# Kernel tuning notes

Hardware: AMD Instinct MI355X
Metric: run time of the kernel (lower is better)

The kernel has to match this reference:

```python
import jax, jax.numpy as jnp
import numpy as np

NUM_GROUPS = 8   # num_groups1, recursive_index=False path
NUM_HEADS = 8


def setup_inputs() -> dict:
    key = jax.random.key(0)
    k1, k2, k3 = jax.random.split(key, 3)
    B, C, H, W = 4, 256, 64, 64
    x = jax.random.normal(k1, (B, C, H, W), dtype=jnp.float32)
    w_qkv = jax.random.normal(k2, (3 * C, C), dtype=jnp.float32) * 0.02
    w_proj = jax.random.normal(k3, (C, C), dtype=jnp.float32) * 0.02
    b_proj = jnp.zeros((C,), dtype=jnp.float32)
    return {"x": x, "w_qkv": w_qkv, "w_proj": w_proj, "b_proj": b_proj}


def reference(x, w_qkv, w_proj, b_proj):
    B, C, H, W = x.shape
    N = H * W
    G = NUM_GROUPS
    nh = NUM_HEADS
    hd = C // nh
    M = N // G
    scale = hd ** -0.5

    # b c h w -> b (h w) c
    xf = x.reshape(B, C, N).transpose(0, 2, 1)  # [B, N, C]

    # qkv linear (no bias), then split into groups / heads
    qkv = (xf @ w_qkv.T).reshape(B, G, M, 3, nh, hd)
    qkv = jnp.transpose(qkv, (3, 0, 1, 4, 2, 5))  # [3, B, G, nh, M, hd]
    q, k, v = qkv[0], qkv[1], qkv[2]

    # grouped multi-head attention, manual softmax
    attn = jax.nn.softmax(jnp.einsum('bghmd,bghnd->bghmn', q, k) * scale, axis=-1)
    out = jnp.einsum('bghmn,bghnd->bghmd', attn, v)

    # [B,G,nh,M,hd] -> [B,G,M,C] -> [B,N,C]
    out = out.transpose(0, 1, 3, 2, 4).reshape(B, N, C)

    out = out @ w_proj.T + b_proj

    # b (h w) c -> b c h w
    return out.transpose(0, 2, 1).reshape(B, C, H, W)
```

## Files before the change

### kernel.cpp

```cpp
#include <hip/hip_runtime.h>
#include <hip/hip_bf16.h>

#define Bb 4
#define Cc 256
#define Nn 4096
#define Gg 8
#define NHh 8
#define HDd 32
#define Mm 512

typedef __bf16 bf16_t;
typedef __bf16 bf16x2 __attribute__((ext_vector_type(2)));
typedef __bf16 bf16x8 __attribute__((ext_vector_type(8)));
typedef __bf16 bf16x4 __attribute__((ext_vector_type(4)));
typedef float f32x4 __attribute__((ext_vector_type(4)));

__device__ __forceinline__ void load_lds16(const bf16_t* g, bf16_t* l) {
  __builtin_amdgcn_global_load_lds(
      (const __attribute__((address_space(1))) void*)g,
      (__attribute__((address_space(3))) void*)l, 16, 0, 0);
}

__global__ __launch_bounds__(256) void prep_kernel(
    const float* __restrict__ x, bf16_t* __restrict__ xT,
    const float* __restrict__ wqkv, const float* __restrict__ wproj,
    bf16_t* __restrict__ wq_b, bf16_t* __restrict__ wp_b) {
  int bid = blockIdx.x, tid = threadIdx.x;
  if (bid >= 1024) {
    int i = (bid - 1024) * 256 + tid;
    wq_b[i] = (bf16_t)wqkv[i];
    if (i < Cc * Cc) wp_b[i] = (bf16_t)wproj[i];
    return;
  }
  __shared__ float t[64][65];
  int b = bid >> 8, c0 = ((bid >> 6) & 3) * 64, n0 = (bid & 63) * 64;
  const float* xp = x + ((long long)b * Cc + c0) * Nn + n0;
  for (int i = tid; i < 4096; i += 256) {
    int r = i >> 6, cc = i & 63;
    t[r][cc] = xp[(long long)r * Nn + cc];
  }
  __syncthreads();
  bf16_t* op = xT + ((long long)b * Nn + n0) * Cc + c0;
  for (int i = tid; i < 2048; i += 256) {
    int r = i >> 5, cc = (i & 31) * 2;
    bf16x2 w;
    w[0] = (bf16_t)t[cc][r];
    w[1] = (bf16_t)t[cc + 1][r];
    *(bf16x2*)&op[(long long)r * Cc + cc] = w;
  }
}

template <int MODE>
__global__ __launch_bounds__(256) void gemm_nt_kernel(
    const bf16_t* __restrict__ A, const bf16_t* __restrict__ Bt,
    void* __restrict__ C0, void* __restrict__ C1,
    const float* __restrict__ bias,
    int M, int N, int K, long long sB, long long sC) {
  __shared__ bf16_t As[128 * 32];
  __shared__ bf16_t Bs[128 * 32];
  int tid = threadIdx.x, lane = tid & 63, wid = tid >> 6;
  int quad = lane >> 4, l16 = lane & 15;
  int z = blockIdx.z;
  if (MODE != 1) Bt += sB * z;
  int m0 = blockIdx.y * 128, n0 = blockIdx.x * 128;
  int wm = (wid >> 1) * 64, wn = (wid & 1) * 64;

  f32x4 acc[4][4];
#pragma unroll
  for (int i = 0; i < 4; ++i)
#pragma unroll
    for (int j = 0; j < 4; ++j) acc[i][j] = (f32x4){0.f, 0.f, 0.f, 0.f};

  int scol = (lane & 3) * 8;
  for (int k0 = 0; k0 < K; k0 += 32) {
    __syncthreads();
#pragma unroll
    for (int r = 0; r < 2; ++r) {
      int chunk = wid * 2 + r;
      int row = chunk * 16 + (lane >> 2);
      load_lds16(&A[(long long)(m0 + row) * K + k0 + scol], &As[chunk * 512]);
      load_lds16(&Bt[(long long)(n0 + row) * K + k0 + scol], &Bs[chunk * 512]);
    }
    __syncthreads();
    bf16x8 a[4], b[4];
#pragma unroll
    for (int i = 0; i < 4; ++i)
      a[i] = *(const bf16x8*)&As[(wm + i * 16 + l16) * 32 + quad * 8];
#pragma unroll
    for (int j = 0; j < 4; ++j)
      b[j] = *(const bf16x8*)&Bs[(wn + j * 16 + l16) * 32 + quad * 8];
#pragma unroll
    for (int i = 0; i < 4; ++i)
#pragma unroll
      for (int j = 0; j < 4; ++j)
        acc[i][j] = __builtin_amdgcn_mfma_f32_16x16x32_bf16(a[i], b[j], acc[i][j], 0, 0, 0);
  }

#pragma unroll
  for (int i = 0; i < 4; ++i) {
#pragma unroll
    for (int j = 0; j < 4; ++j) {
      int col = n0 + wn + j * 16 + l16;
#pragma unroll
      for (int r = 0; r < 4; ++r) {
        int row = m0 + wm + i * 16 + quad * 4 + r;
        float v = acc[i][j][r];
        if (MODE == 1) {
          int b = row >> 12, g = (row >> 9) & 7, m = row & 511;
          int h = (col >> 5) & 7, d = col & 31;
          long long hb = (long long)((b << 6) | (g << 3) | h) * (Mm * HDd);
          if (col < 256)
            ((bf16_t*)C0)[hb + m * HDd + d] = (bf16_t)v;
          else
            ((bf16_t*)C1)[hb + m * HDd + d] = (bf16_t)v;
        } else if (MODE == 3) {
          int hh = row >> 5, d = row & 31, gg = col >> 9, m = col & 511;
          long long hb = (long long)((z << 6) | (gg << 3) | hh) * (Mm * HDd);
          ((bf16_t*)C0)[hb + d * Mm + m] = (bf16_t)v;
        } else {
          ((float*)C0)[sC * z + (long long)row * N + col] = v + bias[row];
        }
      }
    }
  }
}

__global__ __launch_bounds__(256, 2) void attn_kernel(
    const bf16_t* __restrict__ Qh, const bf16_t* __restrict__ Kh,
    const bf16_t* __restrict__ Vh, bf16_t* __restrict__ Oa) {
  __shared__ bf16_t Vs[32 * 520];
  int gid = blockIdx.x;
  int ms = gid & 1, head = gid >> 1;
  int h = head & 7, g = (head >> 3) & 7, b = head >> 6;
  int tid = threadIdx.x, lane = tid & 63, wid = tid >> 6;
  int quad = lane >> 4, l16 = lane & 15;
  const float ls = 0.17677669529663687f * 1.44269504088896340f;

  const bf16_t* Kg = Kh + (long long)head * (Mm * HDd);
  const bf16_t* Vg = Vh + (long long)head * (Mm * HDd);
  const bf16_t* Qg = Qh + (long long)head * (Mm * HDd) + ms * 256 * HDd;

#pragma unroll
  for (int it = 0; it < 8; ++it) {
    int d = wid * 8 + it;
    load_lds16(&Vg[d * Mm + lane * 8], &Vs[d * 520]);
  }
  __syncthreads();

  int rp0 = ((l16 >> 2) << 3) | (l16 & 3);
  const bf16_t* Kp0 = Kg + rp0 * HDd + quad * 8;
  const bf16_t* Kp1 = Kp0 + 4 * HDd;
  const bf16_t* VsL = &Vs[l16 * 520 + quad * 8];
  const bf16_t* VsH = &Vs[(16 + l16) * 520 + quad * 8];
  const f32x4 zero = (f32x4){0.f, 0.f, 0.f, 0.f};

#pragma unroll 1
  for (int t = 0; t < 4; ++t) {
    int m0 = wid * 64 + t * 16;
    bf16x8 qf = *(const bf16x8*)&Qg[(m0 + l16) * HDd + quad * 8];

    float sm = 0.f;
    f32x4 oL = zero, oH = zero;

#pragma unroll 4
    for (int c = 0; c < 16; ++c) {
      int nb = c * 32;
      bf16x8 kf0 = *(const bf16x8*)&Kp0[nb * HDd];
      bf16x8 kf1 = *(const bf16x8*)&Kp1[nb * HDd];
      f32x4 st0 = __builtin_amdgcn_mfma_f32_16x16x32_bf16(kf0, qf, zero, 0, 0, 0);
      f32x4 st1 = __builtin_amdgcn_mfma_f32_16x16x32_bf16(kf1, qf, zero, 0, 0, 0);
      bf16x8 pb;
#pragma unroll
      for (int r = 0; r < 4; ++r) {
        float e = __builtin_exp2f(st0[r] * ls);
        sm += e;
        pb[r] = (bf16_t)e;
      }
#pragma unroll
      for (int r = 0; r < 4; ++r) {
        float e = __builtin_exp2f(st1[r] * ls);
        sm += e;
        pb[4 + r] = (bf16_t)e;
      }
      bf16x8 vL = *(const bf16x8*)&VsL[nb];
      bf16x8 vH = *(const bf16x8*)&VsH[nb];
      oL = __builtin_amdgcn_mfma_f32_16x16x32_bf16(vL, pb, oL, 0, 0, 0);
      oH = __builtin_amdgcn_mfma_f32_16x16x32_bf16(vH, pb, oH, 0, 0, 0);
    }

    sm += __shfl_xor(sm, 16, 64);
    sm += __shfl_xor(sm, 32, 64);
    float inv = 1.f / sm;

    long long orow =
        ((long long)(b * Nn + g * Mm + ms * 256 + m0 + l16)) * Cc + h * HDd;
    bf16x4 wL, wH;
#pragma unroll
    for (int r = 0; r < 4; ++r) {
      wL[r] = (bf16_t)(oL[r] * inv);
      wH[r] = (bf16_t)(oH[r] * inv);
    }
    *(bf16x4*)&Oa[orow + quad * 4] = wL;
    *(bf16x4*)&Oa[orow + 16 + quad * 4] = wH;
  }
}

extern "C" void kernel_launch(void* const* d_in, const int* in_sizes, int n_in,
                              void* d_out, int out_size, void* d_ws, size_t ws_size,
                              hipStream_t stream) {
  (void)in_sizes; (void)n_in; (void)out_size; (void)ws_size;
  const float* x = (const float*)d_in[0];
  const float* w_qkv = (const float*)d_in[1];
  const float* w_proj = (const float*)d_in[2];
  const float* b_proj = (const float*)d_in[3];
  float* out = (float*)d_out;

  char* ws = (char*)d_ws;
  bf16_t* xT  = (bf16_t*)(ws);
  bf16_t* wqb = (bf16_t*)(ws + 8388608);
  bf16_t* wpb = (bf16_t*)(ws + 8781824);
  bf16_t* Qh  = (bf16_t*)(ws + 8912896);
  bf16_t* Kh  = (bf16_t*)(ws + 17301504);
  bf16_t* Vh  = (bf16_t*)(ws + 25690112);
  bf16_t* Oa  = (bf16_t*)(ws + 34078720);

  prep_kernel<<<1792, 256, 0, stream>>>(x, xT, w_qkv, w_proj, wqb, wpb);
  gemm_nt_kernel<1><<<dim3(4, 128, 1), 256, 0, stream>>>(
      xT, wqb, Qh, Kh, nullptr, Bb * Nn, 512, Cc, 0, 0);
  gemm_nt_kernel<3><<<dim3(32, 2, 4), 256, 0, stream>>>(
      wqb + 512 * Cc, xT, Vh, nullptr, nullptr, Cc, Nn, Cc,
      (long long)Nn * Cc, 0);
  attn_kernel<<<512, 256, 0, stream>>>(Qh, Kh, Vh, Oa);
  gemm_nt_kernel<2><<<dim3(32, 2, 4), 256, 0, stream>>>(
      wpb, Oa, out, nullptr, b_proj, Cc, Nn, Cc,
      (long long)Nn * Cc, (long long)Cc * Nn);
}
```

Measured before the change: 134.4 us.

## Merge QK and V GEMMs, fold softmax scale into Q, process two query tiles per wave

The separate QK and V projection GEMM launches become one 768-block kernel, which removes a launch and lets the two tile sets share the GPU. The softmax scale and log2(e) factor are now applied once when Q is written, so the attention inner loop no longer multiplies every score. The attention kernel now handles two 16-row query tiles per iteration, reusing each K fragment and V LDS read across both, at the cost of more accumulator registers. Rounding the scaled Q to bf16 slightly changes numerics.

```diff
diff --git a/kernel.cpp b/kernel.cpp
--- a/kernel.cpp
+++ b/kernel.cpp
@@ -11,9 +11,11 @@
 
 typedef __bf16 bf16_t;
 typedef __bf16 bf16x2 __attribute__((ext_vector_type(2)));
+typedef __bf16 bf16x4 __attribute__((ext_vector_type(4)));
 typedef __bf16 bf16x8 __attribute__((ext_vector_type(8)));
-typedef __bf16 bf16x4 __attribute__((ext_vector_type(4)));
 typedef float f32x4 __attribute__((ext_vector_type(4)));
+
+#define LSCALE (0.17677669529663687f * 1.44269504088896340f)
 
 __device__ __forceinline__ void load_lds16(const bf16_t* g, bf16_t* l) {
   __builtin_amdgcn_global_load_lds(
@@ -50,19 +52,31 @@
   }
 }
 
-template <int MODE>
-__global__ __launch_bounds__(256) void gemm_nt_kernel(
-    const bf16_t* __restrict__ A, const bf16_t* __restrict__ Bt,
-    void* __restrict__ C0, void* __restrict__ C1,
-    const float* __restrict__ bias,
-    int M, int N, int K, long long sB, long long sC) {
+__global__ __launch_bounds__(256) void qkv_gemm_kernel(
+    const bf16_t* __restrict__ xT, const bf16_t* __restrict__ wqb,
+    bf16_t* __restrict__ Qh, bf16_t* __restrict__ Kh, bf16_t* __restrict__ Vh) {
   __shared__ bf16_t As[128 * 32];
   __shared__ bf16_t Bs[128 * 32];
+  int bid = blockIdx.x;
   int tid = threadIdx.x, lane = tid & 63, wid = tid >> 6;
   int quad = lane >> 4, l16 = lane & 15;
-  int z = blockIdx.z;
-  if (MODE != 1) Bt += sB * z;
-  int m0 = blockIdx.y * 128, n0 = blockIdx.x * 128;
+  bool isQK = bid < 512;
+  const bf16_t *A, *Bt;
+  int m0, n0, z = 0;
+  if (isQK) {
+    m0 = (bid >> 2) * 128;
+    n0 = (bid & 3) * 128;
+    A = xT;
+    Bt = wqb;
+  } else {
+    int vb = bid - 512;
+    z = vb >> 6;
+    int rem = vb & 63;
+    m0 = (rem >> 5) * 128;
+    n0 = (rem & 31) * 128;
+    A = wqb + 512 * Cc;
+    Bt = xT + (long long)z * Nn * Cc;
+  }
   int wm = (wid >> 1) * 64, wn = (wid & 1) * 64;
 
   f32x4 acc[4][4];
@@ -72,14 +86,14 @@
     for (int j = 0; j < 4; ++j) acc[i][j] = (f32x4){0.f, 0.f, 0.f, 0.f};
 
   int scol = (lane & 3) * 8;
-  for (int k0 = 0; k0 < K; k0 += 32) {
+  for (int k0 = 0; k0 < Cc; k0 += 32) {
     __syncthreads();
 #pragma unroll
     for (int r = 0; r < 2; ++r) {
       int chunk = wid * 2 + r;
       int row = chunk * 16 + (lane >> 2);
-      load_lds16(&A[(long long)(m0 + row) * K + k0 + scol], &As[chunk * 512]);
-      load_lds16(&Bt[(long long)(n0 + row) * K + k0 + scol], &Bs[chunk * 512]);
+      load_lds16(&A[(long long)(m0 + row) * Cc + k0 + scol], &As[chunk * 512]);
+      load_lds16(&Bt[(long long)(n0 + row) * Cc + k0 + scol], &Bs[chunk * 512]);
     }
     __syncthreads();
     bf16x8 a[4], b[4];
@@ -105,20 +119,18 @@
       for (int r = 0; r < 4; ++r) {
         int row = m0 + wm + i * 16 + quad * 4 + r;
         float v = acc[i][j][r];
-        if (MODE == 1) {
-          int b = row >> 12, g = (row >> 9) & 7, m = row & 511;
-          int h = (col >> 5) & 7, d = col & 31;
-          long long hb = (long long)((b << 6) | (g << 3) | h) * (Mm * HDd);
+        if (isQK) {
+          int bb = row >> 12, gg = (row >> 9) & 7, m = row & 511;
+          int hh = (col >> 5) & 7, d = col & 31;
+          long long hb = (long long)((bb << 6) | (gg << 3) | hh) * (Mm * HDd);
           if (col < 256)
-            ((bf16_t*)C0)[hb + m * HDd + d] = (bf16_t)v;
+            Qh[hb + m * HDd + d] = (bf16_t)(v * LSCALE);
           else
-            ((bf16_t*)C1)[hb + m * HDd + d] = (bf16_t)v;
-        } else if (MODE == 3) {
+            Kh[hb + m * HDd + d] = (bf16_t)v;
+        } else {
           int hh = row >> 5, d = row & 31, gg = col >> 9, m = col & 511;
           long long hb = (long long)((z << 6) | (gg << 3) | hh) * (Mm * HDd);
-          ((bf16_t*)C0)[hb + d * Mm + m] = (bf16_t)v;
-        } else {
-          ((float*)C0)[sC * z + (long long)row * N + col] = v + bias[row];
+          Vh[hb + d * Mm + m] = (bf16_t)v;
         }
       }
     }
@@ -134,7 +146,6 @@
   int h = head & 7, g = (head >> 3) & 7, b = head >> 6;
   int tid = threadIdx.x, lane = tid & 63, wid = tid >> 6;
   int quad = lane >> 4, l16 = lane & 15;
-  const float ls = 0.17677669529663687f * 1.44269504088896340f;
 
   const bf16_t* Kg = Kh + (long long)head * (Mm * HDd);
   const bf16_t* Vg = Vh + (long long)head * (Mm * HDd);
@@ -155,53 +166,124 @@
   const f32x4 zero = (f32x4){0.f, 0.f, 0.f, 0.f};
 
 #pragma unroll 1
-  for (int t = 0; t < 4; ++t) {
-    int m0 = wid * 64 + t * 16;
-    bf16x8 qf = *(const bf16x8*)&Qg[(m0 + l16) * HDd + quad * 8];
-
-    float sm = 0.f;
-    f32x4 oL = zero, oH = zero;
+  for (int t = 0; t < 2; ++t) {
+    int m0 = wid * 64 + t * 32;
+    bf16x8 qa = *(const bf16x8*)&Qg[(m0 + l16) * HDd + quad * 8];
+    bf16x8 qb = *(const bf16x8*)&Qg[(m0 + 16 + l16) * HDd + quad * 8];
+
+    float sma = 0.f, smb = 0.f;
+    f32x4 oLa = zero, oHa = zero, oLb = zero, oHb = zero;
 
 #pragma unroll 4
     for (int c = 0; c < 16; ++c) {
       int nb = c * 32;
       bf16x8 kf0 = *(const bf16x8*)&Kp0[nb * HDd];
       bf16x8 kf1 = *(const bf16x8*)&Kp1[nb * HDd];
-      f32x4 st0 = __builtin_amdgcn_mfma_f32_16x16x32_bf16(kf0, qf, zero, 0, 0, 0);
-      f32x4 st1 = __builtin_amdgcn_mfma_f32_16x16x32_bf16(kf1, qf, zero, 0, 0, 0);
-      bf16x8 pb;
+      f32x4 sa0 = __builtin_amdgcn_mfma_f32_16x16x32_bf16(kf0, qa, zero, 0, 0, 0);
+      f32x4 sa1 = __builtin_amdgcn_mfma_f32_16x16x32_bf16(kf1, qa, zero, 0, 0, 0);
+      f32x4 sb0 = __builtin_amdgcn_mfma_f32_16x16x32_bf16(kf0, qb, zero, 0, 0, 0);
+      f32x4 sb1 = __builtin_amdgcn_mfma_f32_16x16x32_bf16(kf1, qb, zero, 0, 0, 0);
+      bf16x8 pa, pb;
 #pragma unroll
       for (int r = 0; r < 4; ++r) {
-        float e = __builtin_exp2f(st0[r] * ls);
-        sm += e;
-        pb[r] = (bf16_t)e;
-      }
-#pragma unroll
-      for (int r = 0; r < 4; ++r) {
-        float e = __builtin_exp2f(st1[r] * ls);
-        sm += e;
-        pb[4 + r] = (bf16_t)e;
+        float e0 = __builtin_exp2f(sa0[r]);
+        float e1 = __builtin_exp2f(sa1[r]);
+        sma += e0 + e1;
+        pa[r] = (bf16_t)e0;
+        pa[4 + r] = (bf16_t)e1;
+        float f0 = __builtin_exp2f(sb0[r]);
+        float f1 = __builtin_exp2f(sb1[r]);
+        smb += f0 + f1;
+        pb[r] = (bf16_t)f0;
+        pb[4 + r] = (bf16_t)f1;
       }
       bf16x8 vL = *(const bf16x8*)&VsL[nb];
       bf16x8 vH = *(const bf16x8*)&VsH[nb];
-      oL = __builtin_amdgcn_mfma_f32_16x16x32_bf16(vL, pb, oL, 0, 0, 0);
-      oH = __builtin_amdgcn_mfma_f32_16x16x32_bf16(vH, pb, oH, 0, 0, 0);
-    }
-
-    sm += __shfl_xor(sm, 16, 64);
-    sm += __shfl_xor(sm, 32, 64);
-    float inv = 1.f / sm;
-
-    long long orow =
+      oLa = __builtin_amdgcn_mfma_f32_16x16x32_bf16(vL, pa, oLa, 0, 0, 0);
+      oHa = __builtin_amdgcn_mfma_f32_16x16x32_bf16(vH, pa, oHa, 0, 0, 0);
+      oLb = __builtin_amdgcn_mfma_f32_16x16x32_bf16(vL, pb, oLb, 0, 0, 0);
+      oHb = __builtin_amdgcn_mfma_f32_16x16x32_bf16(vH, pb, oHb, 0, 0, 0);
+    }
+
+    sma += __shfl_xor(sma, 16, 64);
+    sma += __shfl_xor(sma, 32, 64);
+    smb += __shfl_xor(smb, 16, 64);
+    smb += __shfl_xor(smb, 32, 64);
+    float inva = 1.f / sma, invb = 1.f / smb;
+
+    long long orowa =
         ((long long)(b * Nn + g * Mm + ms * 256 + m0 + l16)) * Cc + h * HDd;
-    bf16x4 wL, wH;
+    long long orowb = orowa + 16 * Cc;
+    bf16x4 wLa, wHa, wLb, wHb;
 #pragma unroll
     for (int r = 0; r < 4; ++r) {
-      wL[r] = (bf16_t)(oL[r] * inv);
-      wH[r] = (bf16_t)(oH[r] * inv);
-    }
-    *(bf16x4*)&Oa[orow + quad * 4] = wL;
-    *(bf16x4*)&Oa[orow + 16 + quad * 4] = wH;
+      wLa[r] = (bf16_t)(oLa[r] * inva);
+      wHa[r] = (bf16_t)(oHa[r] * inva);
+      wLb[r] = (bf16_t)(oLb[r] * invb);
+      wHb[r] = (bf16_t)(oHb[r] * invb);
+    }
+    *(bf16x4*)&Oa[orowa + quad * 4] = wLa;
+    *(bf16x4*)&Oa[orowa + 16 + quad * 4] = wHa;
+    *(bf16x4*)&Oa[orowb + quad * 4] = wLb;
+    *(bf16x4*)&Oa[orowb + 16 + quad * 4] = wHb;
+  }
+}
+
+__global__ __launch_bounds__(256) void proj_kernel(
+    const bf16_t* __restrict__ Wp, const bf16_t* __restrict__ Oa,
+    float* __restrict__ out, const float* __restrict__ bias) {
+  __shared__ bf16_t As[128 * 32];
+  __shared__ bf16_t Bs[128 * 32];
+  int tid = threadIdx.x, lane = tid & 63, wid = tid >> 6;
+  int quad = lane >> 4, l16 = lane & 15;
+  int z = blockIdx.z;
+  const bf16_t* Bt = Oa + (long long)z * Nn * Cc;
+  int m0 = blockIdx.y * 128, n0 = blockIdx.x * 128;
+  int wm = (wid >> 1) * 64, wn = (wid & 1) * 64;
+
+  f32x4 acc[4][4];
+#pragma unroll
+  for (int i = 0; i < 4; ++i)
+#pragma unroll
+    for (int j = 0; j < 4; ++j) acc[i][j] = (f32x4){0.f, 0.f, 0.f, 0.f};
+
+  int scol = (lane & 3) * 8;
+  for (int k0 = 0; k0 < Cc; k0 += 32) {
+    __syncthreads();
+#pragma unroll
+    for (int r = 0; r < 2; ++r) {
+      int chunk = wid * 2 + r;
+      int row = chunk * 16 + (lane >> 2);
+      load_lds16(&Wp[(long long)(m0 + row) * Cc + k0 + scol], &As[chunk * 512]);
+      load_lds16(&Bt[(long long)(n0 + row) * Cc + k0 + scol], &Bs[chunk * 512]);
+    }
+    __syncthreads();
+    bf16x8 a[4], b[4];
+#pragma unroll
+    for (int i = 0; i < 4; ++i)
+      a[i] = *(const bf16x8*)&As[(wm + i * 16 + l16) * 32 + quad * 8];
+#pragma unroll
+    for (int j = 0; j < 4; ++j)
+      b[j] = *(const bf16x8*)&Bs[(wn + j * 16 + l16) * 32 + quad * 8];
+#pragma unroll
+    for (int i = 0; i < 4; ++i)
+#pragma unroll
+      for (int j = 0; j < 4; ++j)
+        acc[i][j] = __builtin_amdgcn_mfma_f32_16x16x32_bf16(a[i], b[j], acc[i][j], 0, 0, 0);
+  }
+
+#pragma unroll
+  for (int i = 0; i < 4; ++i) {
+#pragma unroll
+    for (int j = 0; j < 4; ++j) {
+      int col = n0 + wn + j * 16 + l16;
+#pragma unroll
+      for (int r = 0; r < 4; ++r) {
+        int row = m0 + wm + i * 16 + quad * 4 + r;
+        out[(long long)z * (Cc * Nn) + (long long)row * Nn + col] =
+            acc[i][j][r] + bias[row];
+      }
+    }
   }
 }
 
@@ -225,13 +307,7 @@
   bf16_t* Oa  = (bf16_t*)(ws + 34078720);
 
   prep_kernel<<<1792, 256, 0, stream>>>(x, xT, w_qkv, w_proj, wqb, wpb);
-  gemm_nt_kernel<1><<<dim3(4, 128, 1), 256, 0, stream>>>(
-      xT, wqb, Qh, Kh, nullptr, Bb * Nn, 512, Cc, 0, 0);
-  gemm_nt_kernel<3><<<dim3(32, 2, 4), 256, 0, stream>>>(
-      wqb + 512 * Cc, xT, Vh, nullptr, nullptr, Cc, Nn, Cc,
-      (long long)Nn * Cc, 0);
+  qkv_gemm_kernel<<<768, 256, 0, stream>>>(xT, wqb, Qh, Kh, Vh);
   attn_kernel<<<512, 256, 0, stream>>>(Qh, Kh, Vh, Oa);
-  gemm_nt_kernel<2><<<dim3(32, 2, 4), 256, 0, stream>>>(
-      wpb, Oa, out, nullptr, b_proj, Cc, Nn, Cc,
-      (long long)Nn * Cc, (long long)Cc * Nn);
-}
+  proj_kernel<<<dim3(32, 2, 4), 256, 0, stream>>>(wpb, Oa, out, b_proj);
+}
```

New measurement: 131.0 us. 2.6% less time.
